# Performance work log

Hardware: AMD Instinct MI355X
Metric: run time of the kernel (lower is better)

## Reference

```python
import jax, jax.numpy as jnp
import numpy as np
from jax import lax

N_FREE = 10
DT = 0.1
COMP = 4


def setup_inputs() -> dict:
    key = jax.random.key(0)
    kx, kw = jax.random.split(key)
    B, D = 256, 16384
    nodes = D // COMP  # 4096
    x = jax.random.normal(kx, (B, D), dtype=jnp.float32)
    # Hopfield-style node-coupling matrix (learned parameter), small init for stable relaxation
    W = jax.random.normal(kw, (nodes, nodes), dtype=jnp.float32) * 0.02
    return {"x": x, "W": W}


def reference(x, W):
    B, D = x.shape
    nodes = D // COMP
    # project scalar features to multivectors (B, nodes, comp)
    x_mv = x.reshape(B, nodes, COMP)
    W_sym = 0.5 * (W + W.T)  # symmetric coupling => well-defined energy

    def step(h, _):
        rho = jnp.tanh(h)                                      # (B, nodes, comp)
        drive = jnp.einsum('nm,bmc->bnc', W_sym, rho) + x_mv   # recurrent + input coupling
        grad_E = h - (1.0 - rho * rho) * drive                 # dE/dh
        return h - DT * grad_E, None

    h_free, _ = lax.scan(step, x_mv, None, length=N_FREE)
    return h_free[..., 0]  # scalar (grade-0) component, (B, nodes)
```

## Files before the change

kernel.cpp:

```cpp
#include <hip/hip_runtime.h>
#include <hip/hip_bf16.h>


#define BATCH   256
#define NODES   4096
#define MDIM    1024
#define KDIM    4096
#define DLEN    16384

typedef __attribute__((ext_vector_type(8))) __bf16 bf16x8;
typedef __attribute__((ext_vector_type(4))) float  f32x4;

static __device__ __forceinline__ unsigned short f32_to_bf16(float f) {
    unsigned int u = __float_as_uint(f);
    u += 0x7fffu + ((u >> 16) & 1u);
    return (unsigned short)(u >> 16);
}

__global__ __launch_bounds__(256)
void symw_kernel(const float* __restrict__ W, unsigned short* __restrict__ Wb) {
    __shared__ float Ta[64][64];
    __shared__ float Tb[64][65];
    const int tn = blockIdx.y, tm = blockIdx.x;
    const int c  = threadIdx.x & 63;
    const int r0 = threadIdx.x >> 6;
#pragma unroll
    for (int rr = 0; rr < 16; ++rr) {
        int r = r0 * 16 + rr;
        Ta[r][c] = W[(size_t)(tn * 64 + r) * 4096 + tm * 64 + c];
        Tb[r][c] = W[(size_t)(tm * 64 + r) * 4096 + tn * 64 + c];
    }
    __syncthreads();
#pragma unroll
    for (int rr = 0; rr < 16; ++rr) {
        int r = r0 * 16 + rr;
        float v = 0.5f * (Ta[r][c] + Tb[c][r]);
        Wb[(size_t)(tn * 64 + r) * 4096 + tm * 64 + c] = f32_to_bf16(v);
    }
}

__global__ __launch_bounds__(256)
void init_kernel(const float* __restrict__ x, float* __restrict__ h,
                 unsigned short* __restrict__ R0) {
    int idx = blockIdx.x * blockDim.x + threadIdx.x;
    int b = idx >> 12;
    int m = idx & 4095;
    f32x4 xv = *(const f32x4*)(x + (size_t)idx * 4);
    *(f32x4*)(h + (size_t)idx * 4) = xv;
#pragma unroll
    for (int c = 0; c < 4; ++c) {
        R0[((size_t)(b * 4 + c)) * (size_t)KDIM + m] = f32_to_bf16(tanhf(xv[c]));
    }
}

#define BM 64
#define BN 128
#define BK 64
#define NT (KDIM / BK)

__global__ __launch_bounds__(256, 2)
void step_kernel(const unsigned short* __restrict__ Rcur,
                 const unsigned short* __restrict__ Wb,
                 const float* __restrict__ x,
                 float* __restrict__ h,
                 unsigned short* __restrict__ Rnxt,
                 float* __restrict__ out) {
    __shared__ unsigned short As[3][BM * BK];
    __shared__ unsigned short Bs[3][BN * BK];

    const int tid  = threadIdx.x;
    const int bx   = blockIdx.x;
    const int by   = blockIdx.y;
    const int rowA0 = by * BM;
    const int rowB0 = bx * BN;

    const int w    = tid >> 6;
    const int lane = tid & 63;
    const int m0   = (w >> 1) * 32;
    const int n0   = (w & 1) * 64;
    const int lr   = lane & 15;
    const int lk   = lane >> 4;

    size_t offA[2], offB[4];
    int ldsoA[2], ldsoB[4];
#pragma unroll
    for (int j = 0; j < 2; ++j) {
        int chunk = tid + 256 * j;
        int row = chunk >> 3, cs = chunk & 7;
        int cg = cs ^ (row & 7);
        offA[j]  = (size_t)(rowA0 + row) * KDIM + cg * 8;
        ldsoA[j] = chunk * 8;
    }
#pragma unroll
    for (int j = 0; j < 4; ++j) {
        int chunk = tid + 256 * j;
        int row = chunk >> 3, cs = chunk & 7;
        int cg = cs ^ (row & 7);
        offB[j]  = (size_t)(rowB0 + row) * KDIM + cg * 8;
        ldsoB[j] = chunk * 8;
    }

    f32x4 acc[2][4];
#pragma unroll
    for (int mi = 0; mi < 2; ++mi)
#pragma unroll
        for (int ni = 0; ni < 4; ++ni)
            acc[mi][ni] = (f32x4){0.f, 0.f, 0.f, 0.f};

#define STAGE(buf, k0)                                                          \
    do {                                                                        \
        _Pragma("unroll")                                                       \
        for (int j = 0; j < 2; ++j) {                                           \
            __builtin_amdgcn_global_load_lds(                                   \
                (const __attribute__((address_space(1))) void*)(Rcur + offA[j] + (k0)), \
                (__attribute__((address_space(3))) void*)(As[buf] + ldsoA[j]),  \
                16, 0, 0);                                                      \
        }                                                                       \
        _Pragma("unroll")                                                       \
        for (int j = 0; j < 4; ++j) {                                           \
            __builtin_amdgcn_global_load_lds(                                   \
                (const __attribute__((address_space(1))) void*)(Wb + offB[j] + (k0)), \
                (__attribute__((address_space(3))) void*)(Bs[buf] + ldsoB[j]),  \
                16, 0, 0);                                                      \
        }                                                                       \
    } while (0)

#define COMPUTE(buf)                                                            \
    do {                                                                        \
        _Pragma("unroll")                                                       \
        for (int kk = 0; kk < 2; ++kk) {                                        \
            bf16x8 a[2], b[4];                                                  \
            _Pragma("unroll")                                                   \
            for (int mi = 0; mi < 2; ++mi) {                                    \
                int row = m0 + mi * 16 + lr;                                    \
                int slot = (kk * 4 + lk) ^ (row & 7);                           \
                a[mi] = *(const bf16x8*)(As[buf] + row * BK + slot * 8);        \
            }                                                                   \
            _Pragma("unroll")                                                   \
            for (int ni = 0; ni < 4; ++ni) {                                    \
                int row = n0 + ni * 16 + lr;                                    \
                int slot = (kk * 4 + lk) ^ (row & 7);                           \
                b[ni] = *(const bf16x8*)(Bs[buf] + row * BK + slot * 8);        \
            }                                                                   \
            _Pragma("unroll")                                                   \
            for (int mi = 0; mi < 2; ++mi)                                      \
                _Pragma("unroll")                                               \
                for (int ni = 0; ni < 4; ++ni)                                  \
                    acc[mi][ni] = __builtin_amdgcn_mfma_f32_16x16x32_bf16(      \
                        a[mi], b[ni], acc[mi][ni], 0, 0, 0);                    \
        }                                                                       \
    } while (0)

    STAGE(0, 0);
    STAGE(1, BK);

    int cur = 0, nxt = 1, far = 2;
    for (int t = 0; t < NT; ++t) {
        if (t == NT - 1) {
            asm volatile("s_waitcnt vmcnt(0)" ::: "memory");
        } else {
            asm volatile("s_waitcnt vmcnt(6)" ::: "memory");
        }
        __builtin_amdgcn_s_barrier();
        if (t + 2 < NT) STAGE(far, (size_t)(t + 2) * BK);
        COMPUTE(cur);
        int tmp = cur; cur = nxt; nxt = far; far = tmp;
    }
#undef STAGE
#undef COMPUTE

#pragma unroll
    for (int mi = 0; mi < 2; ++mi) {
        int i0 = rowA0 + m0 + mi * 16 + lk * 4;
        int b  = i0 >> 2;
#pragma unroll
        for (int ni = 0; ni < 4; ++ni) {
            int n = rowB0 + n0 + ni * 16 + lr;
            size_t hidx = (size_t)b * DLEN + (size_t)n * 4;
            f32x4 h4 = *(const f32x4*)(h + hidx);
            f32x4 x4 = *(const f32x4*)(x + hidx);
            f32x4 hn;
#pragma unroll
            for (int r = 0; r < 4; ++r) {
                float hv   = h4[r];
                float rho  = tanhf(hv);
                float drive = acc[mi][ni][r] + x4[r];
                float hnew = 0.9f * hv + 0.1f * (1.0f - rho * rho) * drive;
                hn[r] = hnew;
                Rnxt[(size_t)(i0 + r) * KDIM + n] = f32_to_bf16(tanhf(hnew));
            }
            *(f32x4*)(h + hidx) = hn;
            if (out) out[(size_t)b * NODES + n] = hn[0];
        }
    }
}

extern "C" void kernel_launch(void* const* d_in, const int* in_sizes, int n_in,
                              void* d_out, int out_size, void* d_ws, size_t ws_size,
                              hipStream_t stream) {
    const float* x = (const float*)d_in[0];
    const float* W = (const float*)d_in[1];
    float* out = (float*)d_out;

    char* ws = (char*)d_ws;
    unsigned short* Wb = (unsigned short*)(ws);
    unsigned short* R0 = (unsigned short*)(ws + ((size_t)32 << 20));
    unsigned short* R1 = (unsigned short*)(ws + ((size_t)40 << 20));
    float*          h  = (float*)(ws + ((size_t)48 << 20));

    symw_kernel<<<dim3(64, 64), 256, 0, stream>>>(W, Wb);
    init_kernel<<<dim3(4096), 256, 0, stream>>>(x, h, R0);

    unsigned short* rc = R0;
    unsigned short* rn = R1;
    for (int s = 0; s < 10; ++s) {
        step_kernel<<<dim3(32, 16), 256, 0, stream>>>(
            rc, Wb, x, h, rn, (s == 9) ? out : nullptr);
        unsigned short* t = rc; rc = rn; rn = t;
    }
}
```

Baseline: 643.0 us.

## Store rho in MFMA-fragment-packed layout and load A operand directly to registers

The tanh activation buffer is now written in a layout packed to match the MFMA A-fragment order. Each lane can then load its A operands straight from global memory into registers, which removes the A tile from LDS staging and the LDS reads that went with it. The epilogue transposes the new rho values through an LDS tile so the packed layout is written with coalesced 16-byte stores. The main loop is unrolled by two so that A register sets alternate while B stays triple-buffered in LDS. The trade-off is direct global loads on the critical path and an extra LDS pass plus barrier in the epilogue.

```diff
diff --git a/kernel.cpp b/kernel.cpp
--- a/kernel.cpp
+++ b/kernel.cpp
@@ -2,11 +2,14 @@
 #include <hip/hip_bf16.h>
 
 
-#define BATCH   256
-#define NODES   4096
-#define MDIM    1024
-#define KDIM    4096
-#define DLEN    16384
+#define NODES 4096
+#define KDIM  4096
+#define DLEN  16384
+#define BM 64
+#define BN 128
+#define BK 64
+#define NT (KDIM / BK)
+#define PSTEP 65536
 
 typedef __attribute__((ext_vector_type(8))) __bf16 bf16x8;
 typedef __attribute__((ext_vector_type(4))) float  f32x4;
@@ -41,37 +44,33 @@
 
 __global__ __launch_bounds__(256)
 void init_kernel(const float* __restrict__ x, float* __restrict__ h,
-                 unsigned short* __restrict__ R0) {
+                 unsigned short* __restrict__ P0) {
     int idx = blockIdx.x * blockDim.x + threadIdx.x;
     int b = idx >> 12;
     int m = idx & 4095;
     f32x4 xv = *(const f32x4*)(x + (size_t)idx * 4);
     *(f32x4*)(h + (size_t)idx * 4) = xv;
+    size_t base = ((size_t)(m >> 5) * 64 + (b >> 2)) * 512
+                + (size_t)((m >> 3) & 3) * 128 + (m & 7);
 #pragma unroll
     for (int c = 0; c < 4; ++c) {
-        R0[((size_t)(b * 4 + c)) * (size_t)KDIM + m] = f32_to_bf16(tanhf(xv[c]));
-    }
-}
-
-#define BM 64
-#define BN 128
-#define BK 64
-#define NT (KDIM / BK)
+        P0[base + (size_t)((b & 3) * 4 + c) * 8] = f32_to_bf16(tanhf(xv[c]));
+    }
+}
 
 __global__ __launch_bounds__(256, 2)
-void step_kernel(const unsigned short* __restrict__ Rcur,
+void step_kernel(const unsigned short* __restrict__ Pcur,
                  const unsigned short* __restrict__ Wb,
                  const float* __restrict__ x,
                  float* __restrict__ h,
-                 unsigned short* __restrict__ Rnxt,
+                 unsigned short* __restrict__ Pnxt,
                  float* __restrict__ out) {
-    __shared__ unsigned short As[3][BM * BK];
     __shared__ unsigned short Bs[3][BN * BK];
+    __shared__ unsigned short Tp[64][136];
 
     const int tid  = threadIdx.x;
     const int bx   = blockIdx.x;
     const int by   = blockIdx.y;
-    const int rowA0 = by * BM;
     const int rowB0 = bx * BN;
 
     const int w    = tid >> 6;
@@ -80,17 +79,10 @@
     const int n0   = (w & 1) * 64;
     const int lr   = lane & 15;
     const int lk   = lane >> 4;
-
-    size_t offA[2], offB[4];
-    int ldsoA[2], ldsoB[4];
-#pragma unroll
-    for (int j = 0; j < 2; ++j) {
-        int chunk = tid + 256 * j;
-        int row = chunk >> 3, cs = chunk & 7;
-        int cg = cs ^ (row & 7);
-        offA[j]  = (size_t)(rowA0 + row) * KDIM + cg * 8;
-        ldsoA[j] = chunk * 8;
-    }
+    const int mr0  = by * 4 + (m0 >> 4);
+
+    size_t offB[4];
+    int    ldsoB[4];
 #pragma unroll
     for (int j = 0; j < 4; ++j) {
         int chunk = tid + 256 * j;
@@ -99,6 +91,12 @@
         offB[j]  = (size_t)(rowB0 + row) * KDIM + cg * 8;
         ldsoB[j] = chunk * 8;
     }
+    size_t offa[2][2];
+#pragma unroll
+    for (int mi = 0; mi < 2; ++mi)
+#pragma unroll
+        for (int kk = 0; kk < 2; ++kk)
+            offa[mi][kk] = (size_t)kk * 32768 + (size_t)(mr0 + mi) * 512 + lane * 8;
 
     f32x4 acc[2][4];
 #pragma unroll
@@ -107,75 +105,95 @@
         for (int ni = 0; ni < 4; ++ni)
             acc[mi][ni] = (f32x4){0.f, 0.f, 0.f, 0.f};
 
-#define STAGE(buf, k0)                                                          \
+    bf16x8 aA[2][2], aB[2][2];
+    unsigned short* Bs0 = &Bs[0][0];
+
+#define STAGE(buf, t)                                                           \
     do {                                                                        \
-        _Pragma("unroll")                                                       \
-        for (int j = 0; j < 2; ++j) {                                           \
-            __builtin_amdgcn_global_load_lds(                                   \
-                (const __attribute__((address_space(1))) void*)(Rcur + offA[j] + (k0)), \
-                (__attribute__((address_space(3))) void*)(As[buf] + ldsoA[j]),  \
-                16, 0, 0);                                                      \
-        }                                                                       \
         _Pragma("unroll")                                                       \
         for (int j = 0; j < 4; ++j) {                                           \
             __builtin_amdgcn_global_load_lds(                                   \
-                (const __attribute__((address_space(1))) void*)(Wb + offB[j] + (k0)), \
-                (__attribute__((address_space(3))) void*)(Bs[buf] + ldsoB[j]),  \
+                (const __attribute__((address_space(1))) void*)                \
+                    (Wb + offB[j] + (size_t)(t) * BK),                          \
+                (__attribute__((address_space(3))) void*)                      \
+                    (Bs0 + (buf) * (BN * BK) + ldsoB[j]),                       \
                 16, 0, 0);                                                      \
         }                                                                       \
     } while (0)
 
-#define COMPUTE(buf)                                                            \
+#define LOADA(aset, t)                                                          \
     do {                                                                        \
+        const unsigned short* Pt = Pcur + (size_t)(t) * PSTEP;                  \
+        _Pragma("unroll")                                                       \
+        for (int mi = 0; mi < 2; ++mi)                                          \
+            _Pragma("unroll")                                                   \
+            for (int kk = 0; kk < 2; ++kk)                                      \
+                aset[mi][kk] = *(const bf16x8*)(Pt + offa[mi][kk]);             \
+    } while (0)
+
+#define COMPUTE(buf, aset)                                                      \
+    do {                                                                        \
+        const unsigned short* Bb = Bs0 + (buf) * (BN * BK);                     \
         _Pragma("unroll")                                                       \
         for (int kk = 0; kk < 2; ++kk) {                                        \
-            bf16x8 a[2], b[4];                                                  \
-            _Pragma("unroll")                                                   \
-            for (int mi = 0; mi < 2; ++mi) {                                    \
-                int row = m0 + mi * 16 + lr;                                    \
-                int slot = (kk * 4 + lk) ^ (row & 7);                           \
-                a[mi] = *(const bf16x8*)(As[buf] + row * BK + slot * 8);        \
-            }                                                                   \
+            bf16x8 bfr[4];                                                      \
             _Pragma("unroll")                                                   \
             for (int ni = 0; ni < 4; ++ni) {                                    \
                 int row = n0 + ni * 16 + lr;                                    \
                 int slot = (kk * 4 + lk) ^ (row & 7);                           \
-                b[ni] = *(const bf16x8*)(Bs[buf] + row * BK + slot * 8);        \
+                bfr[ni] = *(const bf16x8*)(Bb + row * BK + slot * 8);           \
             }                                                                   \
             _Pragma("unroll")                                                   \
             for (int mi = 0; mi < 2; ++mi)                                      \
                 _Pragma("unroll")                                               \
                 for (int ni = 0; ni < 4; ++ni)                                  \
                     acc[mi][ni] = __builtin_amdgcn_mfma_f32_16x16x32_bf16(      \
-                        a[mi], b[ni], acc[mi][ni], 0, 0, 0);                    \
+                        aset[mi][kk], bfr[ni], acc[mi][ni], 0, 0, 0);           \
         }                                                                       \
     } while (0)
 
     STAGE(0, 0);
-    STAGE(1, BK);
-
-    int cur = 0, nxt = 1, far = 2;
-    for (int t = 0; t < NT; ++t) {
-        if (t == NT - 1) {
-            asm volatile("s_waitcnt vmcnt(0)" ::: "memory");
-        } else {
-            asm volatile("s_waitcnt vmcnt(6)" ::: "memory");
-        }
+    LOADA(aA, 0);
+    STAGE(1, 1);
+    LOADA(aB, 1);
+
+    int rc = 0, rn = 1, rf = 2;
+    for (int tp = 0; tp < 31; ++tp) {
+        const int t = tp * 2;
+        asm volatile("s_waitcnt vmcnt(8)" ::: "memory");
         __builtin_amdgcn_s_barrier();
-        if (t + 2 < NT) STAGE(far, (size_t)(t + 2) * BK);
-        COMPUTE(cur);
-        int tmp = cur; cur = nxt; nxt = far; far = tmp;
-    }
+        STAGE(rf, t + 2);
+        COMPUTE(rc, aA);
+        LOADA(aA, t + 2);
+        { int z = rc; rc = rn; rn = rf; rf = z; }
+        asm volatile("s_waitcnt vmcnt(8)" ::: "memory");
+        __builtin_amdgcn_s_barrier();
+        STAGE(rf, t + 3);
+        COMPUTE(rc, aB);
+        LOADA(aB, t + 3);
+        { int z = rc; rc = rn; rn = rf; rf = z; }
+    }
+    asm volatile("s_waitcnt vmcnt(8)" ::: "memory");
+    __builtin_amdgcn_s_barrier();
+    COMPUTE(rc, aA);
+    { int z = rc; rc = rn; rn = rf; rf = z; }
+    asm volatile("s_waitcnt vmcnt(0)" ::: "memory");
+    __builtin_amdgcn_s_barrier();
+    COMPUTE(rc, aB);
 #undef STAGE
+#undef LOADA
 #undef COMPUTE
 
+    const int rowA0 = by * BM;
 #pragma unroll
     for (int mi = 0; mi < 2; ++mi) {
-        int i0 = rowA0 + m0 + mi * 16 + lk * 4;
+        int il = m0 + mi * 16 + lk * 4;
+        int i0 = rowA0 + il;
         int b  = i0 >> 2;
 #pragma unroll
         for (int ni = 0; ni < 4; ++ni) {
-            int n = rowB0 + n0 + ni * 16 + lr;
+            int nl = n0 + ni * 16 + lr;
+            int n  = rowB0 + nl;
             size_t hidx = (size_t)b * DLEN + (size_t)n * 4;
             f32x4 h4 = *(const f32x4*)(h + hidx);
             f32x4 x4 = *(const f32x4*)(x + hidx);
@@ -187,11 +205,21 @@
                 float drive = acc[mi][ni][r] + x4[r];
                 float hnew = 0.9f * hv + 0.1f * (1.0f - rho * rho) * drive;
                 hn[r] = hnew;
-                Rnxt[(size_t)(i0 + r) * KDIM + n] = f32_to_bf16(tanhf(hnew));
+                Tp[il + r][nl] = f32_to_bf16(tanhf(hnew));
             }
             *(f32x4*)(h + hidx) = hn;
             if (out) out[(size_t)b * NODES + n] = hn[0];
         }
+    }
+    __syncthreads();
+#pragma unroll
+    for (int q = 0; q < 4; ++q) {
+        int chunk = w * 4 + q;
+        int kcl = chunk >> 2, mrl = chunk & 3;
+        bf16x8 v = *(const bf16x8*)&Tp[mrl * 16 + lr][kcl * 32 + lk * 8];
+        size_t po = ((size_t)(bx * 4 + kcl) * 64 + (by * 4 + mrl)) * 512
+                  + (size_t)lane * 8;
+        *(bf16x8*)(Pnxt + po) = v;
     }
 }
 
@@ -204,18 +232,18 @@
 
     char* ws = (char*)d_ws;
     unsigned short* Wb = (unsigned short*)(ws);
-    unsigned short* R0 = (unsigned short*)(ws + ((size_t)32 << 20));
-    unsigned short* R1 = (unsigned short*)(ws + ((size_t)40 << 20));
+    unsigned short* P0 = (unsigned short*)(ws + ((size_t)32 << 20));
+    unsigned short* P1 = (unsigned short*)(ws + ((size_t)40 << 20));
     float*          h  = (float*)(ws + ((size_t)48 << 20));
 
     symw_kernel<<<dim3(64, 64), 256, 0, stream>>>(W, Wb);
-    init_kernel<<<dim3(4096), 256, 0, stream>>>(x, h, R0);
-
-    unsigned short* rc = R0;
-    unsigned short* rn = R1;
+    init_kernel<<<dim3(4096), 256, 0, stream>>>(x, h, P0);
+
+    unsigned short* pc = P0;
+    unsigned short* pn = P1;
     for (int s = 0; s < 10; ++s) {
         step_kernel<<<dim3(32, 16), 256, 0, stream>>>(
-            rc, Wb, x, h, rn, (s == 9) ? out : nullptr);
-        unsigned short* t = rc; rc = rn; rn = t;
-    }
-}
+            pc, Wb, x, h, pn, (s == 9) ? out : nullptr);
+        unsigned short* t = pc; pc = pn; pn = t;
+    }
+}
```

After: 611.3 us. 4.9% less time.
